# Kernel optimization log

Measured on AMD Instinct MI355X. Metric: run time of the kernel, lower is better.

Reference implementation:

```python
import jax, jax.numpy as jnp
import numpy as np

BATCH = 16384
NNZ = 524288
INPUT_DIM = 30000
OUTPUT_DIM = 300


def setup_inputs() -> dict:
    key = jax.random.key(0)
    k1, k2, k3, k4 = jax.random.split(key, 4)
    sp_rows = jnp.sort(jax.random.randint(k1, (NNZ,), 0, BATCH, dtype=jnp.int32))
    sp_cols = jax.random.randint(k2, (NNZ,), 0, INPUT_DIM, dtype=jnp.int32)
    sp_vals = jax.random.uniform(k3, (NNZ,), dtype=jnp.float32)
    # glorot init for weights, zeros bias (as in the TF module)
    scale = jnp.sqrt(6.0 / (INPUT_DIM + OUTPUT_DIM)).astype(jnp.float32)
    weights = jax.random.uniform(k4, (INPUT_DIM, OUTPUT_DIM), dtype=jnp.float32,
                                 minval=-scale, maxval=scale)
    bias = jnp.zeros((OUTPUT_DIM,), dtype=jnp.float32)
    return {"sp_rows": sp_rows, "sp_cols": sp_cols, "sp_vals": sp_vals,
            "weights": weights, "bias": bias, "batch_size": BATCH}


def reference(sp_rows, sp_cols, sp_vals, weights, bias, batch_size):
    # sparse [batch, input_dim] @ dense [input_dim, output_dim]:
    # gather weight rows per nnz, scale by value, segment-sum into output rows.
    contrib = sp_vals[:, None] * weights[sp_cols]          # [nnz, output_dim]
    dense_vector = jax.ops.segment_sum(contrib, sp_rows,
                                       num_segments=batch_size)  # [batch, output_dim]
    dense_vector = dense_vector + bias
    return jax.nn.relu(dense_vector)
```

## Files before the change

kernel.cpp:

```cpp
#include <hip/hip_runtime.h>

#define OUT_DIM 300
#define SLICES  5
#define SLICE_B 128

typedef _Float16 half8_t __attribute__((ext_vector_type(8)));
typedef unsigned int uint32x4_t __attribute__((ext_vector_type(4)));

__global__ __launch_bounds__(256) void setup5_kernel(
    const int* __restrict__ rows, int* __restrict__ row_ptr,
    const float* __restrict__ w, unsigned char* __restrict__ wf,
    int nnz, int batch, int in_dim, int scat_blocks)
{
    if ((int)blockIdx.x < scat_blocks) {
        int i = blockIdx.x * 256 + threadIdx.x;
        if (i >= nnz) return;
        int r = rows[i];
        int prev = (i == 0) ? -1 : rows[i - 1];
        for (int q = prev + 1; q <= r; ++q) row_ptr[q] = i;
        if (i == nnz - 1)
            for (int q = r + 1; q <= batch; ++q) row_ptr[q] = nnz;
        return;
    }
    int j = ((int)blockIdx.x - scat_blocks) * 256 + threadIdx.x;
    if (j >= in_dim * (SLICES * 8)) return;
    int r   = j / 40;
    int c16 = j - r * 40;
    int s   = c16 >> 3;
    int kc  = c16 & 7;
    int c0  = c16 * 8;
    const float* wr = w + (size_t)r * OUT_DIM + c0;
    float4 f0 = make_float4(0.f, 0.f, 0.f, 0.f);
    float4 f1 = make_float4(0.f, 0.f, 0.f, 0.f);
    if (c0 + 4 <= OUT_DIM) f0 = *(const float4*)wr;
    if (c0 + 8 <= OUT_DIM) f1 = *(const float4*)(wr + 4);
    half8_t h;
    h[0] = (_Float16)f0.x; h[1] = (_Float16)f0.y;
    h[2] = (_Float16)f0.z; h[3] = (_Float16)f0.w;
    h[4] = (_Float16)f1.x; h[5] = (_Float16)f1.y;
    h[6] = (_Float16)f1.z; h[7] = (_Float16)f1.w;
    *(half8_t*)(wf + ((size_t)s * in_dim + r) * SLICE_B + kc * 16) = h;
}

__global__ __launch_bounds__(256) void spmm5(
    const int* __restrict__ row_ptr,
    const int* __restrict__ cols,
    const float* __restrict__ vals,
    const unsigned char* __restrict__ wf,
    const float* __restrict__ bias,
    float* __restrict__ out,
    int batch, int in_dim, int rowgroups)
{
    __shared__ uint2 sh[4][64];

    const int nb  = (int)gridDim.x;
    const int q8  = nb >> 3, rm = nb & 7;
    const int xcd = (int)blockIdx.x & 7;
    const int bi  = (int)blockIdx.x >> 3;
    const int j   = (xcd < rm ? xcd * (q8 + 1)
                              : rm * (q8 + 1) + (xcd - rm) * q8) + bi;
    const int slice = j / rowgroups;
    const int rg    = j - slice * rowgroups;

    const int wave = threadIdx.x >> 6;
    const int lane = threadIdx.x & 63;
    const int row  = rg * 4 + wave;
    if (row >= batch) return;

    const int grp   = lane >> 3;
    const int choff = (lane & 7) * 16;

    const unsigned char* wslice = wf + (size_t)slice * in_dim * SLICE_B;
    __amdgpu_buffer_rsrc_t rsrc = __builtin_amdgcn_make_buffer_rsrc(
        (void*)wslice, (short)0, in_dim * SLICE_B, 0x00020000);

    uint2* shw = sh[wave];
    const int lo = row_ptr[row];
    const int hi = row_ptr[row + 1];

    float a0 = 0.f, a1 = 0.f, a2 = 0.f, a3 = 0.f;
    float a4 = 0.f, a5 = 0.f, a6 = 0.f, a7 = 0.f;

    for (int base = lo; base < hi; base += 64) {
        const int rem = hi - base;
        const int cnt = rem < 64 ? rem : 64;

        uint2 ov;
        if (lane < cnt) {
            ov.x = (unsigned)cols[base + lane] * SLICE_B;
            ov.y = __float_as_uint(vals[base + lane]);
        } else {
            ov.x = 0x40000000u;
            ov.y = 0u;
        }
        shw[lane] = ov;

        const int rr  = (cnt + 7) >> 3;
        const int rrp = (rr + 3) & ~3;
        for (int r0 = 0; r0 < rrp; r0 += 4) {
#pragma unroll
            for (int u = 0; u < 4; ++u) {
                uint2 q = shw[8 * (r0 + u) + grp];
                float v = __uint_as_float(q.y);
                uint32x4_t raw = __builtin_amdgcn_raw_buffer_load_b128(
                    rsrc, (int)(q.x + choff), 0,  1);
                half8_t wv = __builtin_bit_cast(half8_t, raw);
                a0 += v * (float)wv[0];
                a1 += v * (float)wv[1];
                a2 += v * (float)wv[2];
                a3 += v * (float)wv[3];
                a4 += v * (float)wv[4];
                a5 += v * (float)wv[5];
                a6 += v * (float)wv[6];
                a7 += v * (float)wv[7];
            }
        }
    }

    a0 += __shfl_down(a0, 32); a1 += __shfl_down(a1, 32);
    a2 += __shfl_down(a2, 32); a3 += __shfl_down(a3, 32);
    a4 += __shfl_down(a4, 32); a5 += __shfl_down(a5, 32);
    a6 += __shfl_down(a6, 32); a7 += __shfl_down(a7, 32);
    a0 += __shfl_down(a0, 16); a1 += __shfl_down(a1, 16);
    a2 += __shfl_down(a2, 16); a3 += __shfl_down(a3, 16);
    a4 += __shfl_down(a4, 16); a5 += __shfl_down(a5, 16);
    a6 += __shfl_down(a6, 16); a7 += __shfl_down(a7, 16);
    a0 += __shfl_down(a0, 8);  a1 += __shfl_down(a1, 8);
    a2 += __shfl_down(a2, 8);  a3 += __shfl_down(a3, 8);
    a4 += __shfl_down(a4, 8);  a5 += __shfl_down(a5, 8);
    a6 += __shfl_down(a6, 8);  a7 += __shfl_down(a7, 8);

    if (lane < 8) {
        const int col = slice * 64 + lane * 8;
        if (col + 4 <= OUT_DIM) {
            float* orow = out + (size_t)row * OUT_DIM + col;
            const float4 b0 = *(const float4*)(bias + col);
            float4 s0;
            s0.x = fmaxf(a0 + b0.x, 0.f);
            s0.y = fmaxf(a1 + b0.y, 0.f);
            s0.z = fmaxf(a2 + b0.z, 0.f);
            s0.w = fmaxf(a3 + b0.w, 0.f);
            *(float4*)orow = s0;
            if (col + 8 <= OUT_DIM) {
                const float4 b1 = *(const float4*)(bias + col + 4);
                float4 s1;
                s1.x = fmaxf(a4 + b1.x, 0.f);
                s1.y = fmaxf(a5 + b1.y, 0.f);
                s1.z = fmaxf(a6 + b1.z, 0.f);
                s1.w = fmaxf(a7 + b1.w, 0.f);
                *(float4*)(orow + 4) = s1;
            }
        }
    }
}

__global__ __launch_bounds__(256) void row_ptr_scatter(
    const int* __restrict__ rows, int* __restrict__ row_ptr, int nnz, int batch)
{
    int i = blockIdx.x * 256 + threadIdx.x;
    if (i >= nnz) return;
    int r = rows[i];
    int prev = (i == 0) ? -1 : rows[i - 1];
    for (int q = prev + 1; q <= r; ++q) row_ptr[q] = i;
    if (i == nnz - 1)
        for (int q = r + 1; q <= batch; ++q) row_ptr[q] = nnz;
}

__global__ __launch_bounds__(256) void spmm_wave_f32_kernel(
    const int* __restrict__ row_ptr,
    const int* __restrict__ cols,
    const float* __restrict__ vals,
    const float* __restrict__ weights,
    const float* __restrict__ bias,
    float* __restrict__ out,
    int batch)
{
    const int wave = threadIdx.x >> 6;
    const int lane = threadIdx.x & 63;
    const int row  = blockIdx.x * 4 + wave;
    if (row >= batch) return;

    const int lo = row_ptr[row];
    const int hi = row_ptr[row + 1];
    float4 acc0 = make_float4(0.f, 0.f, 0.f, 0.f);
    float4 acc1 = make_float4(0.f, 0.f, 0.f, 0.f);
    const bool tail = (lane < 75 - 64);

    for (int base = lo; base < hi; base += 64) {
        const int rem = hi - base;
        const int cnt = rem < 64 ? rem : 64;
        int   c = 0;
        float v = 0.0f;
        if (lane < cnt) { c = cols[base + lane]; v = vals[base + lane]; }
        const int rounds = (cnt + 7) & ~7;
        for (int k = 0; k < rounds; k += 8) {
#pragma unroll
            for (int u = 0; u < 8; ++u) {
                const int   cc = __shfl(c, k + u);
                const float vv = __shfl(v, k + u);
                const float4* wrow = (const float4*)(weights + (size_t)cc * OUT_DIM);
                float4 w0 = wrow[lane];
                acc0.x += vv * w0.x; acc0.y += vv * w0.y;
                acc0.z += vv * w0.z; acc0.w += vv * w0.w;
                if (tail) {
                    float4 w1 = wrow[64 + lane];
                    acc1.x += vv * w1.x; acc1.y += vv * w1.y;
                    acc1.z += vv * w1.z; acc1.w += vv * w1.w;
                }
            }
        }
    }

    const float4* b4 = (const float4*)bias;
    float4* orow = (float4*)(out + (size_t)row * OUT_DIM);
    float4 b0 = b4[lane];
    float4 r0;
    r0.x = fmaxf(acc0.x + b0.x, 0.f);
    r0.y = fmaxf(acc0.y + b0.y, 0.f);
    r0.z = fmaxf(acc0.z + b0.z, 0.f);
    r0.w = fmaxf(acc0.w + b0.w, 0.f);
    orow[lane] = r0;
    if (tail) {
        float4 b1 = b4[64 + lane];
        float4 r1;
        r1.x = fmaxf(acc1.x + b1.x, 0.f);
        r1.y = fmaxf(acc1.y + b1.y, 0.f);
        r1.z = fmaxf(acc1.z + b1.z, 0.f);
        r1.w = fmaxf(acc1.w + b1.w, 0.f);
        orow[64 + lane] = r1;
    }
}

extern "C" void kernel_launch(void* const* d_in, const int* in_sizes, int n_in,
                              void* d_out, int out_size, void* d_ws, size_t ws_size,
                              hipStream_t stream) {
    const int*   sp_rows = (const int*)d_in[0];
    const int*   sp_cols = (const int*)d_in[1];
    const float* sp_vals = (const float*)d_in[2];
    const float* weights = (const float*)d_in[3];
    const float* bias    = (const float*)d_in[4];
    float* out = (float*)d_out;

    const int nnz    = in_sizes[0];
    const int w_elts = in_sizes[3];
    const int in_dim = w_elts / OUT_DIM;
    const int batch  = out_size / OUT_DIM;

    size_t rp_bytes = (size_t)(batch + 1) * sizeof(int);
    size_t wf_off   = (rp_bytes + 255) & ~(size_t)255;
    size_t need5    = wf_off + (size_t)in_dim * SLICES * SLICE_B + 256;

    int* row_ptr = (int*)d_ws;
    const int rowgroups = (batch + 3) / 4;

    if (ws_size >= need5) {
        unsigned char* wf = (unsigned char*)d_ws + wf_off;
        const int scat_blocks = (nnz + 255) / 256;
        const int rep_blocks  = (in_dim * (SLICES * 8) + 255) / 256;
        setup5_kernel<<<scat_blocks + rep_blocks, 256, 0, stream>>>(
            sp_rows, row_ptr, weights, wf, nnz, batch, in_dim, scat_blocks);
        spmm5<<<rowgroups * SLICES, 256, 0, stream>>>(
            row_ptr, sp_cols, sp_vals, wf, bias, out, batch, in_dim, rowgroups);
    } else {
        row_ptr_scatter<<<(nnz + 255) / 256, 256, 0, stream>>>(
            sp_rows, row_ptr, nnz, batch);
        spmm_wave_f32_kernel<<<(batch + 3) / 4, 256, 0, stream>>>(
            row_ptr, sp_cols, sp_vals, weights, bias, out, batch);
    }
}
```

Measured before the change: 136.8 us.

## Make spmm kernel persistent with software-prefetched next row segment

```diff
diff --git a/kernel.cpp b/kernel.cpp
--- a/kernel.cpp
+++ b/kernel.cpp
@@ -42,7 +42,7 @@
     *(half8_t*)(wf + ((size_t)s * in_dim + r) * SLICE_B + kc * 16) = h;
 }
 
-__global__ __launch_bounds__(256) void spmm5(
+__global__ __launch_bounds__(256, 8) void spmm5p(
     const int* __restrict__ row_ptr,
     const int* __restrict__ cols,
     const float* __restrict__ vals,
@@ -53,105 +53,161 @@
 {
     __shared__ uint2 sh[4][64];
 
-    const int nb  = (int)gridDim.x;
-    const int q8  = nb >> 3, rm = nb & 7;
+    const int items = SLICES * rowgroups;
+    const int q8  = items >> 3, rm = items & 7;
     const int xcd = (int)blockIdx.x & 7;
     const int bi  = (int)blockIdx.x >> 3;
-    const int j   = (xcd < rm ? xcd * (q8 + 1)
-                              : rm * (q8 + 1) + (xcd - rm) * q8) + bi;
-    const int slice = j / rowgroups;
-    const int rg    = j - slice * rowgroups;
-
-    const int wave = threadIdx.x >> 6;
-    const int lane = threadIdx.x & 63;
-    const int row  = rg * 4 + wave;
-    if (row >= batch) return;
-
+    const int bpx = (int)gridDim.x >> 3;
+    const int it_lo = (xcd < rm) ? xcd * (q8 + 1)
+                                 : rm * (q8 + 1) + (xcd - rm) * q8;
+    const int it_hi = it_lo + ((xcd < rm) ? (q8 + 1) : q8);
+
+    const int wave  = threadIdx.x >> 6;
+    const int lane  = threadIdx.x & 63;
     const int grp   = lane >> 3;
     const int choff = (lane & 7) * 16;
-
-    const unsigned char* wslice = wf + (size_t)slice * in_dim * SLICE_B;
-    __amdgpu_buffer_rsrc_t rsrc = __builtin_amdgcn_make_buffer_rsrc(
-        (void*)wslice, (short)0, in_dim * SLICE_B, 0x00020000);
-
     uint2* shw = sh[wave];
-    const int lo = row_ptr[row];
-    const int hi = row_ptr[row + 1];
-
-    float a0 = 0.f, a1 = 0.f, a2 = 0.f, a3 = 0.f;
-    float a4 = 0.f, a5 = 0.f, a6 = 0.f, a7 = 0.f;
-
-    for (int base = lo; base < hi; base += 64) {
-        const int rem = hi - base;
-        const int cnt = rem < 64 ? rem : 64;
-
-        uint2 ov;
+
+    int it = it_lo + bi;
+    if (it >= it_hi) return;
+
+    int slice = it / rowgroups;
+    int rg    = it - slice * rowgroups;
+    int row   = rg * 4 + wave;
+    int lo = 0, hi = 0;
+    if (row < batch) { lo = row_ptr[row]; hi = row_ptr[row + 1]; }
+    uint2 ov;
+    {
+        int cnt = hi - lo; if (cnt > 64) cnt = 64;
         if (lane < cnt) {
-            ov.x = (unsigned)cols[base + lane] * SLICE_B;
-            ov.y = __float_as_uint(vals[base + lane]);
-        } else {
-            ov.x = 0x40000000u;
-            ov.y = 0u;
-        }
+            ov.x = (unsigned)cols[lo + lane] * SLICE_B;
+            ov.y = __float_as_uint(vals[lo + lane]);
+        } else { ov.x = 0x40000000u; ov.y = 0u; }
+    }
+
+#define FMA8(M, VB)                                            \
+    do {                                                       \
+        float v_ = __uint_as_float(VB);                        \
+        half8_t wv_ = __builtin_bit_cast(half8_t, (M));        \
+        a0 += v_ * (float)wv_[0]; a1 += v_ * (float)wv_[1];    \
+        a2 += v_ * (float)wv_[2]; a3 += v_ * (float)wv_[3];    \
+        a4 += v_ * (float)wv_[4]; a5 += v_ * (float)wv_[5];    \
+        a6 += v_ * (float)wv_[6]; a7 += v_ * (float)wv_[7];    \
+    } while (0)
+
+#define PROCESS(CNT)                                                          \
+    do {                                                                      \
+        uint2 q0 = shw[grp], q1 = shw[grp + 8];                               \
+        uint2 q2 = shw[grp + 16], q3 = shw[grp + 24];                         \
+        uint32x4_t m0 = __builtin_amdgcn_raw_buffer_load_b128(                \
+            rsrc, (int)(q0.x + choff), 0, 1);                                 \
+        uint32x4_t m1 = __builtin_amdgcn_raw_buffer_load_b128(                \
+            rsrc, (int)(q1.x + choff), 0, 1);                                 \
+        uint32x4_t m2 = __builtin_amdgcn_raw_buffer_load_b128(                \
+            rsrc, (int)(q2.x + choff), 0, 1);                                 \
+        uint32x4_t m3 = __builtin_amdgcn_raw_buffer_load_b128(                \
+            rsrc, (int)(q3.x + choff), 0, 1);                                 \
+        FMA8(m0, q0.y); FMA8(m1, q1.y); FMA8(m2, q2.y); FMA8(m3, q3.y);       \
+        if ((CNT) > 32) {                                                     \
+            uint2 q4 = shw[grp + 32], q5 = shw[grp + 40];                     \
+            uint2 q6 = shw[grp + 48], q7 = shw[grp + 56];                     \
+            uint32x4_t m4 = __builtin_amdgcn_raw_buffer_load_b128(            \
+                rsrc, (int)(q4.x + choff), 0, 1);                             \
+            uint32x4_t m5 = __builtin_amdgcn_raw_buffer_load_b128(            \
+                rsrc, (int)(q5.x + choff), 0, 1);                             \
+            uint32x4_t m6 = __builtin_amdgcn_raw_buffer_load_b128(            \
+                rsrc, (int)(q6.x + choff), 0, 1);                             \
+            uint32x4_t m7 = __builtin_amdgcn_raw_buffer_load_b128(            \
+                rsrc, (int)(q7.x + choff), 0, 1);                             \
+            FMA8(m4, q4.y); FMA8(m5, q5.y); FMA8(m6, q6.y); FMA8(m7, q7.y);   \
+        }                                                                     \
+    } while (0)
+
+    while (true) {
+        const int  it_next    = it + bpx;
+        const bool have_next  = it_next < it_hi;
+
+        const unsigned char* wslice = wf + (size_t)slice * in_dim * SLICE_B;
+        __amdgpu_buffer_rsrc_t rsrc = __builtin_amdgcn_make_buffer_rsrc(
+            (void*)wslice, (short)0, in_dim * SLICE_B, 0x00020000);
+
+        int nslice = 0, nrg = 0, nrow = 0, nlo = 0, nhi = 0;
+        if (have_next) {
+            nslice = it_next / rowgroups;
+            nrg    = it_next - nslice * rowgroups;
+            nrow   = nrg * 4 + wave;
+            if (nrow < batch) { nlo = row_ptr[nrow]; nhi = row_ptr[nrow + 1]; }
+        }
+
+        float a0 = 0.f, a1 = 0.f, a2 = 0.f, a3 = 0.f;
+        float a4 = 0.f, a5 = 0.f, a6 = 0.f, a7 = 0.f;
+
+        int cnt0 = hi - lo; if (cnt0 > 64) cnt0 = 64;
         shw[lane] = ov;
-
-        const int rr  = (cnt + 7) >> 3;
-        const int rrp = (rr + 3) & ~3;
-        for (int r0 = 0; r0 < rrp; r0 += 4) {
-#pragma unroll
-            for (int u = 0; u < 4; ++u) {
-                uint2 q = shw[8 * (r0 + u) + grp];
-                float v = __uint_as_float(q.y);
-                uint32x4_t raw = __builtin_amdgcn_raw_buffer_load_b128(
-                    rsrc, (int)(q.x + choff), 0,  1);
-                half8_t wv = __builtin_bit_cast(half8_t, raw);
-                a0 += v * (float)wv[0];
-                a1 += v * (float)wv[1];
-                a2 += v * (float)wv[2];
-                a3 += v * (float)wv[3];
-                a4 += v * (float)wv[4];
-                a5 += v * (float)wv[5];
-                a6 += v * (float)wv[6];
-                a7 += v * (float)wv[7];
+        PROCESS(cnt0);
+
+        for (int base = lo + 64; base < hi; base += 64) {
+            int c2 = hi - base; if (c2 > 64) c2 = 64;
+            uint2 o2;
+            if (lane < c2) {
+                o2.x = (unsigned)cols[base + lane] * SLICE_B;
+                o2.y = __float_as_uint(vals[base + lane]);
+            } else { o2.x = 0x40000000u; o2.y = 0u; }
+            shw[lane] = o2;
+            PROCESS(c2);
+        }
+
+        uint2 nov; nov.x = 0x40000000u; nov.y = 0u;
+        if (have_next) {
+            int ncnt = nhi - nlo; if (ncnt > 64) ncnt = 64;
+            if (lane < ncnt) {
+                nov.x = (unsigned)cols[nlo + lane] * SLICE_B;
+                nov.y = __float_as_uint(vals[nlo + lane]);
             }
         }
-    }
-
-    a0 += __shfl_down(a0, 32); a1 += __shfl_down(a1, 32);
-    a2 += __shfl_down(a2, 32); a3 += __shfl_down(a3, 32);
-    a4 += __shfl_down(a4, 32); a5 += __shfl_down(a5, 32);
-    a6 += __shfl_down(a6, 32); a7 += __shfl_down(a7, 32);
-    a0 += __shfl_down(a0, 16); a1 += __shfl_down(a1, 16);
-    a2 += __shfl_down(a2, 16); a3 += __shfl_down(a3, 16);
-    a4 += __shfl_down(a4, 16); a5 += __shfl_down(a5, 16);
-    a6 += __shfl_down(a6, 16); a7 += __shfl_down(a7, 16);
-    a0 += __shfl_down(a0, 8);  a1 += __shfl_down(a1, 8);
-    a2 += __shfl_down(a2, 8);  a3 += __shfl_down(a3, 8);
-    a4 += __shfl_down(a4, 8);  a5 += __shfl_down(a5, 8);
-    a6 += __shfl_down(a6, 8);  a7 += __shfl_down(a7, 8);
-
-    if (lane < 8) {
-        const int col = slice * 64 + lane * 8;
-        if (col + 4 <= OUT_DIM) {
-            float* orow = out + (size_t)row * OUT_DIM + col;
-            const float4 b0 = *(const float4*)(bias + col);
-            float4 s0;
-            s0.x = fmaxf(a0 + b0.x, 0.f);
-            s0.y = fmaxf(a1 + b0.y, 0.f);
-            s0.z = fmaxf(a2 + b0.z, 0.f);
-            s0.w = fmaxf(a3 + b0.w, 0.f);
-            *(float4*)orow = s0;
-            if (col + 8 <= OUT_DIM) {
-                const float4 b1 = *(const float4*)(bias + col + 4);
-                float4 s1;
-                s1.x = fmaxf(a4 + b1.x, 0.f);
-                s1.y = fmaxf(a5 + b1.y, 0.f);
-                s1.z = fmaxf(a6 + b1.z, 0.f);
-                s1.w = fmaxf(a7 + b1.w, 0.f);
-                *(float4*)(orow + 4) = s1;
+
+        a0 += __shfl_down(a0, 32); a1 += __shfl_down(a1, 32);
+        a2 += __shfl_down(a2, 32); a3 += __shfl_down(a3, 32);
+        a4 += __shfl_down(a4, 32); a5 += __shfl_down(a5, 32);
+        a6 += __shfl_down(a6, 32); a7 += __shfl_down(a7, 32);
+        a0 += __shfl_down(a0, 16); a1 += __shfl_down(a1, 16);
+        a2 += __shfl_down(a2, 16); a3 += __shfl_down(a3, 16);
+        a4 += __shfl_down(a4, 16); a5 += __shfl_down(a5, 16);
+        a6 += __shfl_down(a6, 16); a7 += __shfl_down(a7, 16);
+        a0 += __shfl_down(a0, 8);  a1 += __shfl_down(a1, 8);
+        a2 += __shfl_down(a2, 8);  a3 += __shfl_down(a3, 8);
+        a4 += __shfl_down(a4, 8);  a5 += __shfl_down(a5, 8);
+        a6 += __shfl_down(a6, 8);  a7 += __shfl_down(a7, 8);
+
+        if (lane < 8 && row < batch) {
+            const int col = slice * 64 + lane * 8;
+            if (col + 4 <= OUT_DIM) {
+                float* orow = out + (size_t)row * OUT_DIM + col;
+                const float4 b0 = *(const float4*)(bias + col);
+                float4 s0;
+                s0.x = fmaxf(a0 + b0.x, 0.f);
+                s0.y = fmaxf(a1 + b0.y, 0.f);
+                s0.z = fmaxf(a2 + b0.z, 0.f);
+                s0.w = fmaxf(a3 + b0.w, 0.f);
+                *(float4*)orow = s0;
+                if (col + 8 <= OUT_DIM) {
+                    const float4 b1 = *(const float4*)(bias + col + 4);
+                    float4 s1;
+                    s1.x = fmaxf(a4 + b1.x, 0.f);
+                    s1.y = fmaxf(a5 + b1.y, 0.f);
+                    s1.z = fmaxf(a6 + b1.z, 0.f);
+                    s1.w = fmaxf(a7 + b1.w, 0.f);
+                    *(float4*)(orow + 4) = s1;
+                }
             }
         }
-    }
+
+        if (!have_next) break;
+        it = it_next; slice = nslice; rg = nrg; row = nrow;
+        lo = nlo; hi = nhi; ov = nov;
+    }
+#undef PROCESS
+#undef FMA8
 }
 
 __global__ __launch_bounds__(256) void row_ptr_scatter(
@@ -259,7 +315,7 @@
         const int rep_blocks  = (in_dim * (SLICES * 8) + 255) / 256;
         setup5_kernel<<<scat_blocks + rep_blocks, 256, 0, stream>>>(
             sp_rows, row_ptr, weights, wf, nnz, batch, in_dim, scat_blocks);
-        spmm5<<<rowgroups * SLICES, 256, 0, stream>>>(
+        spmm5p<<<2048, 256, 0, stream>>>(
             row_ptr, sp_cols, sp_vals, wf, bias, out, batch, in_dim, rowgroups);
     } else {
         row_ptr_scatter<<<(nnz + 255) / 256, 256, 0, stream>>>(
```

Result: faster. 133.5 us (-2.4%).
